# Performance work log

Measured on AMD Instinct MI355X. Metric: run time of the kernel, lower is better.

Reference implementation:

```python
import jax, jax.numpy as jnp
import numpy as np

N_NODES = 100000


def setup_inputs() -> dict:
    key = jax.random.key(0)
    ks = jax.random.split(key, 10)
    N, T, IN, H, OUT = N_NODES, 20, 1, 64, 1
    E = 3200000
    s = 1.0 / np.sqrt(H)
    return {
        "x": jax.random.normal(ks[0], (N, T, IN), dtype=jnp.float32),
        "edge_index": jax.random.randint(ks[1], (E, 2), 0, N, dtype=jnp.int64),
        "W_ih": jax.random.uniform(ks[2], (H, IN), jnp.float32, -s, s),
        "b_ih": jax.random.uniform(ks[3], (H,), jnp.float32, -s, s),
        "W_hh": jax.random.uniform(ks[4], (H, H), jnp.float32, -s, s),
        "b_hh": jax.random.uniform(ks[5], (H,), jnp.float32, -s, s),
        "W_gcn": jax.random.uniform(ks[6], (H, H), jnp.float32, -s, s),
        "b_gcn": jax.random.uniform(ks[7], (H,), jnp.float32, -s, s),
        "W_fc": jax.random.uniform(ks[8], (OUT, H), jnp.float32, -s, s),
        "b_fc": jax.random.uniform(ks[9], (OUT,), jnp.float32, -s, s),
    }


def _strnn_fwd(x, edge_index, W_ih, b_ih, W_hh, b_hh, W_gcn, b_gcn, W_fc, b_fc):
    N = x.shape[0]
    H = W_hh.shape[0]

    # ---- vanilla tanh RNN (batch_first); only last hidden state is needed ----
    xs = jnp.swapaxes(x, 0, 1)  # [T, N, in]

    def step(h, xt):
        h = jnp.tanh(xt @ W_ih.T + b_ih + h @ W_hh.T + b_hh)
        return h, None

    h_last, _ = jax.lax.scan(step, jnp.zeros((N, H), x.dtype), xs)  # [N, H]

    # ---- GCNConv: add self-loops, sym-normalize, linear, scatter-add ----
    src = edge_index[:, 0]
    dst = edge_index[:, 1]
    loop = jnp.arange(N, dtype=src.dtype)
    src = jnp.concatenate([src, loop])
    dst = jnp.concatenate([dst, loop])

    xw = h_last @ W_gcn.T  # [N, H]
    deg = jax.ops.segment_sum(jnp.ones_like(dst, dtype=xw.dtype), dst, num_segments=N)
    dinv = jnp.where(deg > 0, jax.lax.rsqrt(deg), 0.0)
    norm = dinv[src] * dinv[dst]  # [E+N]

    msgs = xw[src] * norm[:, None]  # gather + scale, [E+N, H]
    agg = jax.ops.segment_sum(msgs, dst, num_segments=N) + b_gcn  # scatter-add

    return agg @ W_fc.T + b_fc  # [N, out]


def reference(x, edge_index, W_ih, b_ih, W_hh, b_hh, W_gcn, b_gcn, W_fc, b_fc):
    return _strnn_fwd(x, edge_index, W_ih, b_ih, W_hh, b_hh, W_gcn, b_gcn, W_fc, b_fc)
```

## Files before the change

kernel.cpp:

```cpp
#include <hip/hip_runtime.h>

#define TT 20
#define HH 64
#define RSZ 16384
#define DRSZ 16384
#define NSL 64
#define NSLD 32

typedef __attribute__((ext_vector_type(8))) short short8;
typedef __attribute__((ext_vector_type(4))) float f32x4;

__device__ __forceinline__ unsigned fbits(float f) { union { float f; unsigned u; } v; v.f = f; return v.u; }
__device__ __forceinline__ float bcast(unsigned u) { union { float f; unsigned u; } v; v.u = u; return v.f; }

__global__ __launch_bounds__(256, 3) void k_fused(
    const float* __restrict__ x,
    const float* __restrict__ W_ih, const float* __restrict__ b_ih,
    const float* __restrict__ W_hh, const float* __restrict__ b_hh,
    const float* __restrict__ W_gcn, const float* __restrict__ W_fc,
    const int* __restrict__ ei, unsigned* __restrict__ degrep,
    float* __restrict__ z, int N, int E, int RD, int N2)
{
    __shared__ __align__(16) unsigned smem[8192];

    const int t = threadIdx.x;
    const int RDN = RD * NSLD;

    if (blockIdx.x < RDN) {
        unsigned* bin = smem;
        const int r = blockIdx.x % RD;
        const int s = blockIdx.x / RD;
        const int base = r * DRSZ;
        for (int i = t; i < DRSZ / 2; i += 256) bin[i] = 0;
        __syncthreads();
        const long long P = (long long)(E >> 1);
        const long long pb = s * P / NSLD;
        const long long pe = (s + 1) * P / NSLD;
        const int4* ei4 = (const int4*)ei;
        for (long long g = pb + t; g < pe; g += 256) {
            int4 q = ei4[g];
            unsigned u0 = (unsigned)(q.y - base);
            unsigned u1 = (unsigned)(q.w - base);
            if (u0 < DRSZ) atomicAdd(&bin[u0 >> 1], 1u << ((u0 & 1) << 4));
            if (u1 < DRSZ) atomicAdd(&bin[u1 >> 1], 1u << ((u1 & 1) << 4));
        }
        if ((E & 1) && s == NSLD - 1 && t == 0) {
            unsigned u = (unsigned)(ei[2 * (E - 1) + 1] - base);
            if (u < DRSZ) atomicAdd(&bin[u >> 1], 1u << ((u & 1) << 4));
        }
        __syncthreads();
        const int lim = min(DRSZ, N - base);
        const int words = (lim + 1) >> 1;
        unsigned* dst = degrep + (size_t)s * N2 + (base >> 1);
        for (int i = t; i < words; i += 256) dst[i] = bin[i];
        return;
    }

    const int w    = t >> 6;
    const int l    = t & 63;
    const int nl   = l & 15;
    const int quad = l >> 4;
    const int n0   = (blockIdx.x - RDN) * 64 + w * 16;

    unsigned short* hh = (unsigned short*)&smem[w * 512];
    unsigned short* hl = (unsigned short*)&smem[2048 + w * 512];
    float*          sx = (float*)&smem[4096 + w * 320];

    for (int i = l; i < 16 * TT; i += 64) {
        int nn = i / TT, tt = i - nn * TT;
        int n = n0 + nn; if (n >= N) n = N - 1;
        sx[tt * 16 + nn] = x[(size_t)n * TT + tt];
    }
    {
        uint4 zz = {0, 0, 0, 0};
        uint4* ph = (uint4*)hh;
        uint4* pl = (uint4*)hl;
#pragma unroll
        for (int i = 0; i < 2; ++i) { ph[l + 64 * i] = zz; pl[l + 64 * i] = zz; }
    }

    short8 Bh[4][2], Bl[4][2];
#pragma unroll
    for (int tt2 = 0; tt2 < 4; ++tt2)
#pragma unroll
        for (int kc = 0; kc < 2; ++kc) {
            const float* wr = W_hh + (size_t)(16 * tt2 + nl) * HH + kc * 32 + quad * 8;
            float4 w0 = *(const float4*)(wr);
            float4 w1 = *(const float4*)(wr + 4);
            float wvv[8] = {w0.x, w0.y, w0.z, w0.w, w1.x, w1.y, w1.z, w1.w};
            short8 sh, sl;
#pragma unroll
            for (int j = 0; j < 8; ++j) {
                unsigned u  = fbits(wvv[j]);
                unsigned hb = u & 0xffff0000u;
                float lo = wvv[j] - bcast(hb);
                sh[j] = (short)(hb >> 16);
                sl[j] = (short)(fbits(lo) >> 16);
            }
            Bh[tt2][kc] = sh; Bl[tt2][kc] = sl;
        }

    float vl = 0.0f;
#pragma unroll 8
    for (int j = 0; j < HH; ++j) vl = fmaf(W_fc[j], W_gcn[j * HH + l], vl);

    float wih4[4], bs4[4], vv[4];
#pragma unroll
    for (int tt2 = 0; tt2 < 4; ++tt2) {
        int n = nl + 16 * tt2;
        wih4[tt2] = W_ih[n];
        bs4[tt2]  = b_ih[n] + b_hh[n];
        vv[tt2]   = __shfl(vl, n, 64);
    }

    const int ra = (l ^ ((l >> 4) & 1)) * 8;

    f32x4 C[4];

    for (int step = 0; step < TT; ++step) {
        const float4 xr = *(const float4*)&sx[step * 16 + quad * 4];
#pragma unroll
        for (int tt2 = 0; tt2 < 4; ++tt2) {
            C[tt2][0] = fmaf(xr.x, wih4[tt2], bs4[tt2]);
            C[tt2][1] = fmaf(xr.y, wih4[tt2], bs4[tt2]);
            C[tt2][2] = fmaf(xr.z, wih4[tt2], bs4[tt2]);
            C[tt2][3] = fmaf(xr.w, wih4[tt2], bs4[tt2]);
        }

#pragma unroll
        for (int kc = 0; kc < 2; ++kc) {
            short8 Ah = *(const short8*)&hh[kc * 512 + ra];
            short8 Al = *(const short8*)&hl[kc * 512 + ra];
#pragma unroll
            for (int tt2 = 0; tt2 < 4; ++tt2) {
                C[tt2] = __builtin_amdgcn_mfma_f32_16x16x32_bf16(Ah, Bh[tt2][kc], C[tt2], 0, 0, 0);
                C[tt2] = __builtin_amdgcn_mfma_f32_16x16x32_bf16(Ah, Bl[tt2][kc], C[tt2], 0, 0, 0);
                C[tt2] = __builtin_amdgcn_mfma_f32_16x16x32_bf16(Al, Bh[tt2][kc], C[tt2], 0, 0, 0);
            }
        }

#pragma unroll
        for (int tt2 = 0; tt2 < 4; ++tt2) {
            const int kc_d = tt2 >> 1;
            const int qa   = (nl >> 3) + 2 * (tt2 & 1);
            const int jj   = nl & 7;
#pragma unroll
            for (int r = 0; r < 4; ++r) {
                float eg = __builtin_amdgcn_exp2f(C[tt2][r] * 2.885390081777927f);
                float hv = fmaf(-2.0f, __builtin_amdgcn_rcpf(eg + 1.0f), 1.0f);
                C[tt2][r] = hv;
                unsigned um = fbits(hv);
                unsigned hb = um & 0xffff0000u;
                float lo = hv - bcast(hb);
                const int m   = quad * 4 + r;
                const int la  = m + 16 * qa;
                const int idx = kc_d * 512 + (la ^ ((la >> 4) & 1)) * 8 + jj;
                hh[idx] = (unsigned short)(um >> 16);
                hl[idx] = (unsigned short)(fbits(lo) >> 16);
            }
        }
    }

#pragma unroll
    for (int r = 0; r < 4; ++r) {
        float p = 0.0f;
#pragma unroll
        for (int tt2 = 0; tt2 < 4; ++tt2) p = fmaf(C[tt2][r], vv[tt2], p);
        p += __shfl_xor(p, 1, 64);
        p += __shfl_xor(p, 2, 64);
        p += __shfl_xor(p, 4, 64);
        p += __shfl_xor(p, 8, 64);
        if (nl == 0) {
            const int n = n0 + quad * 4 + r;
            if (n < N) z[n] = p;
        }
    }
}

__global__ __launch_bounds__(256) void k_w(const unsigned* __restrict__ degrep,
                                           const float* __restrict__ z,
                                           float* __restrict__ dinv,
                                           float* __restrict__ w, int N, int N2) {
    int n = blockIdx.x * blockDim.x + threadIdx.x;
    if (n >= N) return;
    const int wd = n >> 1, sh = (n & 1) << 4;
    unsigned d = 0;
#pragma unroll 8
    for (int s = 0; s < NSLD; ++s) d += (degrep[(size_t)s * N2 + wd] >> sh) & 0xffffu;
    float di = __frsqrt_rn((float)d + 1.0f);
    dinv[n] = di;
    w[n] = di * z[n];
}

__global__ __launch_bounds__(1024) void k_edge_bin(const int* __restrict__ ei,
                                                   const float* __restrict__ w,
                                                   float* __restrict__ Srep,
                                                   int N, int E, int R) {
    __shared__ float bin[RSZ];
    const int r = blockIdx.x % R;
    const int s = blockIdx.x / R;
    const int base = r * RSZ;
    for (int i = threadIdx.x; i < RSZ; i += 1024) bin[i] = 0.0f;
    __syncthreads();
    const long long P = (long long)(E >> 1);
    const long long pb = s * P / NSL;
    const long long pe = (s + 1) * P / NSL;
    const int4* ei4 = (const int4*)ei;
    for (long long g = pb + threadIdx.x; g < pe; g += 1024) {
        int4 q = ei4[g];
        unsigned u0 = (unsigned)(q.y - base);
        unsigned u1 = (unsigned)(q.w - base);
        if (u0 < RSZ) atomicAdd(&bin[u0], w[q.x]);
        if (u1 < RSZ) atomicAdd(&bin[u1], w[q.z]);
    }
    if ((E & 1) && s == NSL - 1 && threadIdx.x == 0) {
        unsigned u = (unsigned)(ei[2 * (E - 1) + 1] - base);
        if (u < RSZ) atomicAdd(&bin[u], w[ei[2 * (E - 1)]]);
    }
    __syncthreads();
    const int lim = min(RSZ, N - base);
    float* dst = Srep + (size_t)s * N + base;
    for (int i = threadIdx.x; i < lim; i += 1024) dst[i] = bin[i];
}

__global__ __launch_bounds__(256) void k_final(const float* __restrict__ dinv,
                                               const float* __restrict__ Srep,
                                               const float* __restrict__ w,
                                               const float* __restrict__ b_gcn,
                                               const float* __restrict__ W_fc,
                                               const float* __restrict__ b_fc,
                                               float* __restrict__ out, int N)
{
    float c = b_fc[0];
#pragma unroll 8
    for (int j = 0; j < HH; ++j) c = fmaf(W_fc[j], b_gcn[j], c);
    int n = blockIdx.x * blockDim.x + threadIdx.x;
    if (n >= N) return;
    float S = 0.0f;
#pragma unroll 8
    for (int s = 0; s < NSL; ++s) S += Srep[(size_t)s * N + n];
    float d = dinv[n];
    out[n] = fmaf(d, S, fmaf(d, w[n], c));
}

extern "C" void kernel_launch(void* const* d_in, const int* in_sizes, int n_in,
                              void* d_out, int out_size, void* d_ws, size_t ws_size,
                              hipStream_t stream)
{
    const float* x     = (const float*)d_in[0];
    const int*   ei    = (const int*)d_in[1];
    const float* W_ih  = (const float*)d_in[2];
    const float* b_ih  = (const float*)d_in[3];
    const float* W_hh  = (const float*)d_in[4];
    const float* b_hh  = (const float*)d_in[5];
    const float* W_gcn = (const float*)d_in[6];
    const float* b_gcn = (const float*)d_in[7];
    const float* W_fc  = (const float*)d_in[8];
    const float* b_fc  = (const float*)d_in[9];
    float* out = (float*)d_out;

    const int N  = in_sizes[0] / TT;
    const int E  = in_sizes[1] / 2;
    const int N2 = (N + 1) / 2;
    const int RD = (N + DRSZ - 1) / DRSZ;
    const int RS = (N + RSZ - 1) / RSZ;

    char* ws = (char*)d_ws;
    size_t off = 0;
    auto alloc = [&](size_t bytes) { void* p = ws + off; off += (bytes + 255) & ~(size_t)255; return p; };
    unsigned* degrep = (unsigned*)alloc((size_t)NSLD * N2 * 4);
    float*    Srep   = (float*)   alloc((size_t)NSL * N * 4);
    float*    z      = (float*)   alloc((size_t)N * 4);
    float*    dinv   = (float*)   alloc((size_t)N * 4);
    float*    w      = (float*)   alloc((size_t)N * 4);

    const int rnnBlocks = (N + 63) / 64;
    k_fused   <<<RD * NSLD + rnnBlocks, 256, 0, stream>>>(x, W_ih, b_ih, W_hh, b_hh,
                                                          W_gcn, W_fc, ei, degrep,
                                                          z, N, E, RD, N2);
    k_w       <<<(N + 255) / 256, 256, 0, stream>>>(degrep, z, dinv, w, N, N2);
    k_edge_bin<<<RS * NSL, 1024, 0, stream>>>(ei, w, Srep, N, E, RS);
    k_final   <<<(N + 255) / 256, 256, 0, stream>>>(dinv, Srep, w, b_gcn, W_fc, b_fc, out, N);
}
```

Before: 221.2 us.

## Partition edges by destination range during degree pass, reuse partitions for scatter

```diff
diff --git a/kernel.cpp b/kernel.cpp
--- a/kernel.cpp
+++ b/kernel.cpp
@@ -3,9 +3,9 @@
 #define TT 20
 #define HH 64
 #define RSZ 16384
-#define DRSZ 16384
-#define NSL 64
 #define NSLD 32
+#define CAP 18432
+#define SPILLCAP (1 << 18)
 
 typedef __attribute__((ext_vector_type(8))) short short8;
 typedef __attribute__((ext_vector_type(4))) float f32x4;
@@ -13,15 +13,18 @@
 __device__ __forceinline__ unsigned fbits(float f) { union { float f; unsigned u; } v; v.f = f; return v.u; }
 __device__ __forceinline__ float bcast(unsigned u) { union { float f; unsigned u; } v; v.u = u; return v.f; }
 
-__global__ __launch_bounds__(256, 3) void k_fused(
+__global__ __launch_bounds__(256, 4) void k_fused(
     const float* __restrict__ x,
     const float* __restrict__ W_ih, const float* __restrict__ b_ih,
     const float* __restrict__ W_hh, const float* __restrict__ b_hh,
     const float* __restrict__ W_gcn, const float* __restrict__ W_fc,
     const int* __restrict__ ei, unsigned* __restrict__ degrep,
+    unsigned* __restrict__ Part, int* __restrict__ cnt,
+    int* __restrict__ spill, int* __restrict__ spillCur,
     float* __restrict__ z, int N, int E, int RD, int N2)
 {
     __shared__ __align__(16) unsigned smem[8192];
+    __shared__ int scur;
 
     const int t = threadIdx.x;
     const int RDN = RD * NSLD;
@@ -30,8 +33,10 @@
         unsigned* bin = smem;
         const int r = blockIdx.x % RD;
         const int s = blockIdx.x / RD;
-        const int base = r * DRSZ;
-        for (int i = t; i < DRSZ / 2; i += 256) bin[i] = 0;
+        const int base = r * RSZ;
+        unsigned* part = Part + (size_t)((r * NSLD) + s) * CAP;
+        for (int i = t; i < RSZ / 2; i += 256) bin[i] = 0;
+        if (t == 0) scur = 0;
         __syncthreads();
         const long long P = (long long)(E >> 1);
         const long long pb = s * P / NSLD;
@@ -39,20 +44,41 @@
         const int4* ei4 = (const int4*)ei;
         for (long long g = pb + t; g < pe; g += 256) {
             int4 q = ei4[g];
-            unsigned u0 = (unsigned)(q.y - base);
-            unsigned u1 = (unsigned)(q.w - base);
-            if (u0 < DRSZ) atomicAdd(&bin[u0 >> 1], 1u << ((u0 & 1) << 4));
-            if (u1 < DRSZ) atomicAdd(&bin[u1 >> 1], 1u << ((u1 & 1) << 4));
+#pragma unroll
+            for (int h = 0; h < 2; ++h) {
+                int src = h ? q.z : q.x;
+                int dst = h ? q.w : q.y;
+                unsigned u = (unsigned)(dst - base);
+                if (u < RSZ) {
+                    atomicAdd(&bin[u >> 1], 1u << ((u & 1) << 4));
+                    int pos = atomicAdd(&scur, 1);
+                    if (pos < CAP) part[pos] = (u << 18) | (unsigned)src;
+                    else {
+                        int sp = atomicAdd(spillCur, 1);
+                        if (sp < SPILLCAP) { spill[2 * sp] = src; spill[2 * sp + 1] = dst; }
+                    }
+                }
+            }
         }
         if ((E & 1) && s == NSLD - 1 && t == 0) {
-            unsigned u = (unsigned)(ei[2 * (E - 1) + 1] - base);
-            if (u < DRSZ) atomicAdd(&bin[u >> 1], 1u << ((u & 1) << 4));
+            int src = ei[2 * (E - 1)], dst = ei[2 * (E - 1) + 1];
+            unsigned u = (unsigned)(dst - base);
+            if (u < RSZ) {
+                atomicAdd(&bin[u >> 1], 1u << ((u & 1) << 4));
+                int pos = atomicAdd(&scur, 1);
+                if (pos < CAP) part[pos] = (u << 18) | (unsigned)src;
+                else {
+                    int sp = atomicAdd(spillCur, 1);
+                    if (sp < SPILLCAP) { spill[2 * sp] = src; spill[2 * sp + 1] = dst; }
+                }
+            }
         }
         __syncthreads();
-        const int lim = min(DRSZ, N - base);
+        const int lim = min(RSZ, N - base);
         const int words = (lim + 1) >> 1;
-        unsigned* dst = degrep + (size_t)s * N2 + (base >> 1);
-        for (int i = t; i < words; i += 256) dst[i] = bin[i];
+        unsigned* dstp = degrep + (size_t)s * N2 + (base >> 1);
+        for (int i = t; i < words; i += 256) dstp[i] = bin[i];
+        if (t == 0) cnt[r * NSLD + s] = scur;
         return;
     }
 
@@ -192,35 +218,36 @@
     w[n] = di * z[n];
 }
 
-__global__ __launch_bounds__(1024) void k_edge_bin(const int* __restrict__ ei,
-                                                   const float* __restrict__ w,
-                                                   float* __restrict__ Srep,
-                                                   int N, int E, int R) {
+__global__ __launch_bounds__(1024) void k_sbin(const unsigned* __restrict__ Part,
+                                               const int* __restrict__ cnt,
+                                               const float* __restrict__ w,
+                                               float* __restrict__ Srep,
+                                               int N, int RD) {
     __shared__ float bin[RSZ];
-    const int r = blockIdx.x % R;
-    const int s = blockIdx.x / R;
+    const int r = blockIdx.x % RD;
+    const int s = blockIdx.x / RD;
     const int base = r * RSZ;
     for (int i = threadIdx.x; i < RSZ; i += 1024) bin[i] = 0.0f;
     __syncthreads();
-    const long long P = (long long)(E >> 1);
-    const long long pb = s * P / NSL;
-    const long long pe = (s + 1) * P / NSL;
-    const int4* ei4 = (const int4*)ei;
-    for (long long g = pb + threadIdx.x; g < pe; g += 1024) {
-        int4 q = ei4[g];
-        unsigned u0 = (unsigned)(q.y - base);
-        unsigned u1 = (unsigned)(q.w - base);
-        if (u0 < RSZ) atomicAdd(&bin[u0], w[q.x]);
-        if (u1 < RSZ) atomicAdd(&bin[u1], w[q.z]);
-    }
-    if ((E & 1) && s == NSL - 1 && threadIdx.x == 0) {
-        unsigned u = (unsigned)(ei[2 * (E - 1) + 1] - base);
-        if (u < RSZ) atomicAdd(&bin[u], w[ei[2 * (E - 1)]]);
+    const int n = min(cnt[r * NSLD + s], CAP);
+    const unsigned* part = Part + (size_t)((r * NSLD) + s) * CAP;
+    for (int i = threadIdx.x; i < n; i += 1024) {
+        unsigned rec = part[i];
+        atomicAdd(&bin[rec >> 18], w[rec & 0x3ffffu]);
     }
     __syncthreads();
     const int lim = min(RSZ, N - base);
     float* dst = Srep + (size_t)s * N + base;
     for (int i = threadIdx.x; i < lim; i += 1024) dst[i] = bin[i];
+}
+
+__global__ __launch_bounds__(256) void k_spill(const int* __restrict__ spill,
+                                               const int* __restrict__ spillCur,
+                                               const float* __restrict__ w,
+                                               float* __restrict__ Srep) {
+    int m = min(*spillCur, SPILLCAP);
+    for (int i = threadIdx.x; i < m; i += 256)
+        atomicAdd(&Srep[spill[2 * i + 1]], w[spill[2 * i]]);
 }
 
 __global__ __launch_bounds__(256) void k_final(const float* __restrict__ dinv,
@@ -238,7 +265,7 @@
     if (n >= N) return;
     float S = 0.0f;
 #pragma unroll 8
-    for (int s = 0; s < NSL; ++s) S += Srep[(size_t)s * N + n];
+    for (int s = 0; s < NSLD; ++s) S += Srep[(size_t)s * N + n];
     float d = dinv[n];
     out[n] = fmaf(d, S, fmaf(d, w[n], c));
 }
@@ -262,23 +289,30 @@
     const int N  = in_sizes[0] / TT;
     const int E  = in_sizes[1] / 2;
     const int N2 = (N + 1) / 2;
-    const int RD = (N + DRSZ - 1) / DRSZ;
-    const int RS = (N + RSZ - 1) / RSZ;
+    const int RD = (N + RSZ - 1) / RSZ;
 
     char* ws = (char*)d_ws;
     size_t off = 0;
     auto alloc = [&](size_t bytes) { void* p = ws + off; off += (bytes + 255) & ~(size_t)255; return p; };
-    unsigned* degrep = (unsigned*)alloc((size_t)NSLD * N2 * 4);
-    float*    Srep   = (float*)   alloc((size_t)NSL * N * 4);
-    float*    z      = (float*)   alloc((size_t)N * 4);
-    float*    dinv   = (float*)   alloc((size_t)N * 4);
-    float*    w      = (float*)   alloc((size_t)N * 4);
+    unsigned* degrep  = (unsigned*)alloc((size_t)NSLD * N2 * 4);
+    float*    Srep    = (float*)   alloc((size_t)NSLD * N * 4);
+    unsigned* Part    = (unsigned*)alloc((size_t)RD * NSLD * CAP * 4);
+    int*      cnt     = (int*)     alloc((size_t)RD * NSLD * 4);
+    int*      spill   = (int*)     alloc((size_t)SPILLCAP * 8);
+    int*      spillCur= (int*)     alloc(4);
+    float*    z       = (float*)   alloc((size_t)N * 4);
+    float*    dinv    = (float*)   alloc((size_t)N * 4);
+    float*    w       = (float*)   alloc((size_t)N * 4);
+
+    hipMemsetAsync(spillCur, 0, 4, stream);
 
     const int rnnBlocks = (N + 63) / 64;
-    k_fused   <<<RD * NSLD + rnnBlocks, 256, 0, stream>>>(x, W_ih, b_ih, W_hh, b_hh,
-                                                          W_gcn, W_fc, ei, degrep,
-                                                          z, N, E, RD, N2);
-    k_w       <<<(N + 255) / 256, 256, 0, stream>>>(degrep, z, dinv, w, N, N2);
-    k_edge_bin<<<RS * NSL, 1024, 0, stream>>>(ei, w, Srep, N, E, RS);
-    k_final   <<<(N + 255) / 256, 256, 0, stream>>>(dinv, Srep, w, b_gcn, W_fc, b_fc, out, N);
-}
+    k_fused <<<RD * NSLD + rnnBlocks, 256, 0, stream>>>(x, W_ih, b_ih, W_hh, b_hh,
+                                                        W_gcn, W_fc, ei, degrep,
+                                                        Part, cnt, spill, spillCur,
+                                                        z, N, E, RD, N2);
+    k_w     <<<(N + 255) / 256, 256, 0, stream>>>(degrep, z, dinv, w, N, N2);
+    k_sbin  <<<RD * NSLD, 1024, 0, stream>>>(Part, cnt, w, Srep, N, RD);
+    k_spill <<<1, 256, 0, stream>>>(spill, spillCur, w, Srep);
+    k_final <<<(N + 255) / 256, 256, 0, stream>>>(dinv, Srep, w, b_gcn, W_fc, b_fc, out, N);
+}
```

After: 249.2 us. 12.7% more time.
